# Performance work log

Hardware: AMD Instinct MI355X
Metric: run time of the kernel (lower is better)

The kernel has to match this reference:

```python
import jax, jax.numpy as jnp
import numpy as np

WEIGHT = 1.0  # config['weight']


def setup_inputs() -> dict:
    key = jax.random.key(0)
    ks = jax.random.split(key, 10)
    B, N, S, C, D, E, H, V = 8, 4096, 512, 16, 1024, 256, 1024, 100000
    return {
        "span_vecs": jax.random.normal(ks[0], (B, N, D), jnp.float32),
        "ent_table": jax.random.normal(ks[1], (V, E), jnp.float32) * 0.02,
        "W1": jax.random.normal(ks[2], (D + E, H), jnp.float32) * (1.0 / np.sqrt(D + E)),
        "b1": jnp.zeros((H,), jnp.float32),
        "W2": jax.random.normal(ks[3], (H,), jnp.float32) * (1.0 / np.sqrt(H)),
        "b2": jnp.zeros((), jnp.float32),
        "targets_all": jax.random.uniform(ks[4], (B, N, C), jnp.float32),
        "linker_indices": jax.random.randint(ks[5], (B, S), 0, N, jnp.int32),
        "candidates_all": jax.random.randint(ks[6], (B, N, C), 0, V, jnp.int32),
        "candidate_lengths_all": jax.random.randint(ks[7], (B, N), 0, C + 1, jnp.int32),
    }


def reference(span_vecs, ent_table, W1, b1, W2, b2, targets_all,
              linker_indices, candidates_all, candidate_lengths_all):
    D = span_vecs.shape[-1]
    C = candidates_all.shape[-1]
    idx = linker_indices  # [B, S]

    # batched_index_select gathers over the span axis
    candidates = jnp.take_along_axis(candidates_all, idx[:, :, None], axis=1)        # [B,S,C] int
    lengths = jnp.take_along_axis(candidate_lengths_all, idx, axis=1)                # [B,S] int
    targets = jnp.take_along_axis(targets_all, idx[:, :, None], axis=1)              # [B,S,C]
    linker_vecs = jnp.take_along_axis(span_vecs, idx[:, :, None], axis=1)            # [B,S,D]

    cand_vecs = ent_table[candidates]                                                # [B,S,C,E]

    # layers: Linear(D+E,H) -> ReLU -> (dropout=identity in eval) -> Linear(H,1)
    # fused: split W1 so the [B,S,C,D+E] expanded concat is never materialized
    W1s, W1e = W1[:D], W1[D:]
    h_span = jnp.einsum('bsd,dh->bsh', linker_vecs, W1s)                             # [B,S,H]
    h_cand = jnp.einsum('bsce,eh->bsch', cand_vecs, W1e)                             # [B,S,C,H]
    h = jax.nn.relu(h_span[:, :, None, :] + h_cand + b1)
    scores = jnp.einsum('bsch,h->bsc', h, W2) + b2                                   # [B,S,C]

    # create_candidate_mask
    mask = (jnp.arange(C)[None, None, :] < lengths[:, :, None]).astype(scores.dtype)

    # BCEWithLogitsLoss(reduction='none'), masked sum * weight
    bce = jnp.maximum(scores, 0.0) - scores * targets + jnp.log1p(jnp.exp(-jnp.abs(scores)))
    loss = (mask * bce).sum() * WEIGHT

    predictions = jnp.argmax(scores - (1.0 - mask) * 1e23, axis=-1)                  # [B,S]
    return loss, scores, predictions
```

## Files before the change

kernel.cpp:

```cpp
#include <hip/hip_runtime.h>
#include <math.h>


typedef short short8 __attribute__((ext_vector_type(8)));
typedef _Float16 half8v __attribute__((ext_vector_type(8)));
typedef float f32x16 __attribute__((ext_vector_type(16)));

static __device__ inline unsigned short f2bf(float x) {
  unsigned u = __float_as_uint(x);
  unsigned r = (u + 0x7FFFu + ((u >> 16) & 1u)) >> 16;
  return (unsigned short)r;
}
static __device__ inline float bf2f(unsigned short b) {
  return __uint_as_float(((unsigned)b) << 16);
}
static __device__ inline unsigned short f2h(float x) {
  _Float16 h = (_Float16)x;
  return *(unsigned short*)&h;
}

#define GLD_TO_LDS(gp, lp)                                          \
  __builtin_amdgcn_global_load_lds(                                 \
      (const __attribute__((address_space(1))) void*)(gp),          \
      (__attribute__((address_space(3))) void*)(lp), 16, 0, 0)

static __device__ inline void split_write(unsigned short* buf, int g,
                                          float4 c0, float4 c1) {
  float xs[8] = {c0.x, c0.y, c0.z, c0.w, c1.x, c1.y, c1.z, c1.w};
  short8 h8, l8;
#pragma unroll
  for (int j = 0; j < 8; ++j) {
    unsigned short h = f2bf(xs[j]);
    h8[j] = (short)h;
    l8[j] = (short)f2bf(xs[j] - bf2f(h));
  }
  *(short8*)(buf + (g << 3)) = h8;
  *(short8*)(buf + 4096 + (g << 3)) = l8;
}

__global__ __launch_bounds__(256) void k_prep_e(
    const float* __restrict__ ent, const float* __restrict__ W1,
    const int* __restrict__ linker, const int* __restrict__ cand_all,
    unsigned short* __restrict__ A2, unsigned short* __restrict__ sThi,
    unsigned short* __restrict__ sTlo, unsigned short* __restrict__ eT16) {
  __shared__ float t[32][33];
  const int bx = blockIdx.x;
  if (bx < 16384) {
    int f = bx * 256 + threadIdx.x;
    int row = f >> 6;
    int pair = row >> 4;
    int b = pair >> 9;
    int i = linker[pair];
    int cid = cand_all[(((size_t)b << 12) + (size_t)i) * 16 + (row & 15)];
    const float4 v = *((const float4*)(ent + ((size_t)cid << 8)) + (f & 63));
    *(ushort4*)(A2 + ((size_t)f << 2)) =
        make_ushort4(f2h(v.x), f2h(v.y), f2h(v.z), f2h(v.w));
  } else {
    int b2x = bx - 16384;
    int n0 = (b2x & 31) * 32, k0 = (b2x >> 5) * 32;
    int rr = threadIdx.x >> 5, cc = threadIdx.x & 31;
#pragma unroll
    for (int i = 0; i < 4; ++i)
      t[rr + 8 * i][cc] = W1[(size_t)(k0 + rr + 8 * i) * 1024 + n0 + cc];
    __syncthreads();
#pragma unroll
    for (int i = 0; i < 4; ++i) {
      int nl = rr + 8 * i;
      float v = t[cc][nl];
      int n = n0 + nl, k = k0 + cc;
      if (k0 < 1024) {
        unsigned short h = f2bf(v);
        unsigned short l = f2bf(v - bf2f(h));
        sThi[(size_t)n * 1024 + k] = h;
        sTlo[(size_t)n * 1024 + k] = l;
      } else {
        eT16[(size_t)n * 256 + (k - 1024)] = f2h(v);
      }
    }
  }
}

template <int KSTEPS>
__global__ __launch_bounds__(256, 2) void k_g32g(
    const float* __restrict__ span, const int* __restrict__ linker,
    const unsigned short* __restrict__ Bhi, const unsigned short* __restrict__ Blo,
    float* __restrict__ Out) {
  const int tid = threadIdx.x;
  const int l = tid & 63;
  const int w = tid >> 6;
  const int wm = w >> 1, wn = w & 1;
  const int id = blockIdx.x;
  const int z = id >> 8;
  const int sid = id & 255;
  const int m8 = sid & 7;
  const int cb = (sid >> 3) & 7;
  const int q = sid >> 6;
  const int row0 = ((q << 3) + m8) << 7;
  const int col0 = cb << 7;
  const int koff = z * (KSTEPS * 32);
  Out += (size_t)z * 4194304;

  __shared__ unsigned short lds[32768];

  f32x16 acc[2][2];
#pragma unroll
  for (int i = 0; i < 2; ++i)
#pragma unroll
    for (int j = 0; j < 2; ++j)
#pragma unroll
      for (int k = 0; k < 16; ++k) acc[i][j][k] = 0.f;

  const int ar0 = tid >> 2, ap0 = tid & 3;
  const int al0c = ap0 ^ ((ar0 >> 1) & 3);
  const int ar1 = ar0 + 64;
  const int al1c = ap0 ^ ((ar1 >> 1) & 3);
  const int r0g = row0 + ar0, r1g = row0 + ar1;
  const float* asrc0 =
      span + (((size_t)(r0g >> 9) << 12) + linker[r0g]) * 1024 + koff + al0c * 8;
  const float* asrc1 =
      span + (((size_t)(r1g >> 9) << 12) + linker[r1g]) * 1024 + koff + al1c * 8;
  const size_t boff0 = (size_t)(col0 + ar0) * 1024 + al0c * 8 + koff;
  const size_t boff1 = (size_t)(col0 + ar1) * 1024 + al1c * 8 + koff;
  const int w512 = w * 512;

  {
    float4 a00 = *(const float4*)(asrc0);
    float4 a01 = *(const float4*)(asrc0 + 4);
    float4 a10 = *(const float4*)(asrc1);
    float4 a11 = *(const float4*)(asrc1 + 4);
    GLD_TO_LDS(Bhi + boff0, lds + 8192 + w512);
    GLD_TO_LDS(Bhi + boff1, lds + 10240 + w512);
    GLD_TO_LDS(Blo + boff0, lds + 12288 + w512);
    GLD_TO_LDS(Blo + boff1, lds + 14336 + w512);
    split_write(lds, tid, a00, a01);
    split_write(lds, tid + 256, a10, a11);
  }
  asm volatile("s_waitcnt vmcnt(0) lgkmcnt(0)" ::: "memory");
  __builtin_amdgcn_s_barrier();
  asm volatile("" ::: "memory");

  for (int ks = 0; ks < KSTEPS; ++ks) {
    float4 a00, a01, a10, a11;
    const int k0n = (ks + 1) * 32;
    unsigned short* bn = lds + (((ks + 1) & 1) << 14);
    if (ks + 1 < KSTEPS) {
      a00 = *(const float4*)(asrc0 + k0n);
      a01 = *(const float4*)(asrc0 + k0n + 4);
      a10 = *(const float4*)(asrc1 + k0n);
      a11 = *(const float4*)(asrc1 + k0n + 4);
      GLD_TO_LDS(Bhi + boff0 + k0n, bn + 8192 + w512);
      GLD_TO_LDS(Bhi + boff1 + k0n, bn + 10240 + w512);
      GLD_TO_LDS(Blo + boff0 + k0n, bn + 12288 + w512);
      GLD_TO_LDS(Blo + boff1 + k0n, bn + 14336 + w512);
    }

    const unsigned short* cbuf = lds + ((ks & 1) << 14);
#pragma unroll
    for (int kc = 0; kc < 2; ++kc) {
      const int kg = kc * 2 + (l >> 5);
      short8 ah[2], alv[2], bh[2], bl[2];
#pragma unroll
      for (int it = 0; it < 2; ++it) {
        int r = wm * 64 + it * 32 + (l & 31);
        int off = r * 32 + ((kg ^ ((r >> 1) & 3)) << 3);
        ah[it] = *(const short8*)(cbuf + off);
        alv[it] = *(const short8*)(cbuf + 4096 + off);
      }
#pragma unroll
      for (int jt = 0; jt < 2; ++jt) {
        int r = wn * 64 + jt * 32 + (l & 31);
        int off = r * 32 + ((kg ^ ((r >> 1) & 3)) << 3);
        bh[jt] = *(const short8*)(cbuf + 8192 + off);
        bl[jt] = *(const short8*)(cbuf + 12288 + off);
      }
#pragma unroll
      for (int it = 0; it < 2; ++it)
#pragma unroll
        for (int jt = 0; jt < 2; ++jt) {
          acc[it][jt] = __builtin_amdgcn_mfma_f32_32x32x16_bf16(
              ah[it], bh[jt], acc[it][jt], 0, 0, 0);
          acc[it][jt] = __builtin_amdgcn_mfma_f32_32x32x16_bf16(
              ah[it], bl[jt], acc[it][jt], 0, 0, 0);
          acc[it][jt] = __builtin_amdgcn_mfma_f32_32x32x16_bf16(
              alv[it], bh[jt], acc[it][jt], 0, 0, 0);
        }
    }

    if (ks + 1 < KSTEPS) {
      split_write(bn, tid, a00, a01);
      split_write(bn, tid + 256, a10, a11);
      asm volatile("s_waitcnt vmcnt(0) lgkmcnt(0)" ::: "memory");
      __builtin_amdgcn_s_barrier();
      asm volatile("" ::: "memory");
    }
  }

#pragma unroll
  for (int it = 0; it < 2; ++it) {
    int mb = row0 + wm * 64 + it * 32 + 4 * (l >> 5);
#pragma unroll
    for (int jt = 0; jt < 2; ++jt) {
      int n = col0 + wn * 64 + jt * 32 + (l & 31);
#pragma unroll
      for (int rg = 0; rg < 16; ++rg) {
        int m = mb + (rg & 3) + 8 * (rg >> 2);
        Out[(size_t)m * 1024 + n] = acc[it][jt][rg];
      }
    }
  }
}

__global__ __launch_bounds__(256, 4) void k_gf16(
    const unsigned short* __restrict__ A,
    const unsigned short* __restrict__ Bt,
    const float* __restrict__ HsIn, const float* __restrict__ b1,
    const float* __restrict__ W2, float* __restrict__ Out) {
  const int tid = threadIdx.x;
  const int l = tid & 63;
  const int w = tid >> 6;
  const int wm = w >> 1, wn = w & 1;
  const int id = blockIdx.x;
  const int m8 = id & 7;
  const int cb = (id >> 3) & 7;
  const int q = id >> 6;
  const int row0 = ((q << 3) + m8) << 7;
  const int col0 = cb << 7;

  __shared__ unsigned short lds[16384];

  f32x16 acc[2][2];
#pragma unroll
  for (int i = 0; i < 2; ++i)
#pragma unroll
    for (int j = 0; j < 2; ++j)
#pragma unroll
      for (int k = 0; k < 16; ++k) acc[i][j][k] = 0.f;

  const int ar0 = tid >> 2, ap0 = tid & 3;
  const int al0c = ap0 ^ ((ar0 >> 1) & 3);
  const int ar1 = (tid + 256) >> 2;
  const int al1c = ap0 ^ ((ar1 >> 1) & 3);
  const size_t aoff0 = (size_t)(row0 + ar0) * 256 + al0c * 8;
  const size_t aoff1 = (size_t)(row0 + ar1) * 256 + al1c * 8;
  const size_t boff0 = (size_t)(col0 + ar0) * 256 + al0c * 8;
  const size_t boff1 = (size_t)(col0 + ar1) * 256 + al1c * 8;
  const int w512 = w * 512;

  GLD_TO_LDS(A + aoff0, lds + w512);
  GLD_TO_LDS(A + aoff1, lds + 2048 + w512);
  GLD_TO_LDS(Bt + boff0, lds + 4096 + w512);
  GLD_TO_LDS(Bt + boff1, lds + 6144 + w512);
  asm volatile("s_waitcnt vmcnt(0)" ::: "memory");
  __builtin_amdgcn_s_barrier();
  asm volatile("" ::: "memory");

#pragma unroll 2
  for (int ks = 0; ks < 8; ++ks) {
    if (ks + 1 < 8) {
      const int k0 = (ks + 1) * 32;
      unsigned short* b = lds + (((ks + 1) & 1) << 13);
      GLD_TO_LDS(A + aoff0 + k0, b + w512);
      GLD_TO_LDS(A + aoff1 + k0, b + 2048 + w512);
      GLD_TO_LDS(Bt + boff0 + k0, b + 4096 + w512);
      GLD_TO_LDS(Bt + boff1 + k0, b + 6144 + w512);
    }

    const unsigned short* cbuf = lds + ((ks & 1) << 13);
#pragma unroll
    for (int kc = 0; kc < 2; ++kc) {
      const int kg = kc * 2 + (l >> 5);
      half8v av[2], bv[2];
#pragma unroll
      for (int it = 0; it < 2; ++it) {
        int r = wm * 64 + it * 32 + (l & 31);
        int off = r * 32 + ((kg ^ ((r >> 1) & 3)) << 3);
        av[it] = *(const half8v*)(cbuf + off);
      }
#pragma unroll
      for (int jt = 0; jt < 2; ++jt) {
        int r = wn * 64 + jt * 32 + (l & 31);
        int off = r * 32 + ((kg ^ ((r >> 1) & 3)) << 3);
        bv[jt] = *(const half8v*)(cbuf + 4096 + off);
      }
#pragma unroll
      for (int it = 0; it < 2; ++it)
#pragma unroll
        for (int jt = 0; jt < 2; ++jt)
          acc[it][jt] = __builtin_amdgcn_mfma_f32_32x32x16_f16(
              av[it], bv[jt], acc[it][jt], 0, 0, 0);
    }

    if (ks + 1 < 8) {
      asm volatile("s_waitcnt vmcnt(0)" ::: "memory");
      __builtin_amdgcn_s_barrier();
      asm volatile("" ::: "memory");
    }
  }

  float sv[2][16];
#pragma unroll
  for (int it = 0; it < 2; ++it) {
#pragma unroll
    for (int rg = 0; rg < 16; ++rg) sv[it][rg] = 0.f;
    const int p0 = (row0 + wm * 64 + it * 32) >> 4;
#pragma unroll
    for (int jt = 0; jt < 2; ++jt) {
      int n = col0 + wn * 64 + jt * 32 + (l & 31);
      float b1v = b1[n], w2v = W2[n];
      float add0 = HsIn[(size_t)p0 * 1024 + n] +
                   HsIn[4194304 + (size_t)p0 * 1024 + n] + b1v;
      float add1 = HsIn[(size_t)(p0 + 1) * 1024 + n] +
                   HsIn[4194304 + (size_t)(p0 + 1) * 1024 + n] + b1v;
#pragma unroll
      for (int rg = 0; rg < 16; ++rg) {
        float h = fmaxf(acc[it][jt][rg] + (rg < 8 ? add0 : add1), 0.f);
        sv[it][rg] = fmaf(h, w2v, sv[it][rg]);
      }
    }
  }
  __syncthreads();
  float* scf = (float*)lds;
  const int cc0 = l & 31, lh4 = 4 * (l >> 5);
#pragma unroll
  for (int it = 0; it < 2; ++it)
#pragma unroll
    for (int rg = 0; rg < 16; ++rg) {
      int row = (rg & 3) + 8 * (rg >> 2) + lh4;
      scf[((w * 2 + it) * 32 + row) * 32 + ((cc0 + row) & 31)] = sv[it][rg];
    }
  __syncthreads();
  int gr = tid >> 1, h = tid & 1;
  int r = gr & 31, itv = (gr >> 5) & 1, wmv = gr >> 6;
  const float* sa = scf + ((wmv * 4 + itv) * 32 + r) * 32;
  const float* sb = scf + ((wmv * 4 + 2 + itv) * 32 + r) * 32;
  float sum = 0.f;
#pragma unroll
  for (int j = 0; j < 16; ++j) {
    int cidx = (h * 16 + j + r) & 31;
    sum += sa[cidx] + sb[cidx];
  }
  sum += __shfl_xor(sum, 1, 64);
  if (h == 0) Out[(size_t)cb * 65536 + row0 + gr] = sum;
}

__global__ __launch_bounds__(64) void k_final8(const float* __restrict__ score8,
                                               const float* __restrict__ b2p,
                                               const float* __restrict__ targets_all,
                                               const int* __restrict__ linker,
                                               const int* __restrict__ len_all,
                                               float* __restrict__ out) {
  int p = blockIdx.x * 64 + threadIdx.x;
  float b2 = b2p[0];
  int b = p >> 9;
  int i = linker[p];
  int len = len_all[(b << 12) + i];
  const float* tg = targets_all + ((((size_t)b << 12) + (size_t)i) << 4);

  float sc[16];
#pragma unroll
  for (int c = 0; c < 16; ++c) sc[c] = b2;
#pragma unroll
  for (int c8 = 0; c8 < 8; ++c8) {
    const float4* q4 = (const float4*)(score8 + (size_t)c8 * 65536 + p * 16);
#pragma unroll
    for (int j = 0; j < 4; ++j) {
      float4 v = q4[j];
      sc[j * 4 + 0] += v.x; sc[j * 4 + 1] += v.y;
      sc[j * 4 + 2] += v.z; sc[j * 4 + 3] += v.w;
    }
  }

  float loss = 0.f;
  float best = -INFINITY;
  int bc = 0;
#pragma unroll
  for (int c = 0; c < 16; ++c) {
    float s = sc[c];
    out[1 + p * 16 + c] = s;
    float val;
    if (c < len) {
      float t = tg[c];
      loss += fmaxf(s, 0.f) - s * t + log1pf(expf(-fabsf(s)));
      val = s;
    } else {
      val = s - 1e23f;
    }
    if (val > best) { best = val; bc = c; }
  }
  out[1 + 65536 + p] = (float)bc;

  for (int off = 32; off > 0; off >>= 1) loss += __shfl_down(loss, off, 64);
  if (threadIdx.x == 0) atomicAdd(out, loss);
}

#define BM 128
#define BN 128
#define BK 16
#define PAD 4

__global__ __launch_bounds__(256) void k_prep(const int* __restrict__ linker,
                                              const int* __restrict__ cand_all,
                                              int* __restrict__ cand_ids) {
  int g = blockIdx.x * 256 + threadIdx.x;
  int pair = g >> 4;
  int c = g & 15;
  int b = pair >> 9;
  int i = linker[pair];
  cand_ids[g] = cand_all[(((size_t)b << 12) + (size_t)i) * 16 + c];
}

__global__ __launch_bounds__(256) void k_hs(const float* __restrict__ span,
                                            const float* __restrict__ W1,
                                            const int* __restrict__ linker,
                                            float* __restrict__ Hs) {
  const int tid = threadIdx.x;
  const int tx = tid & 15, ty = tid >> 4;
  const int row0 = blockIdx.y * BM;
  const int col0 = blockIdx.x * BN;
  __shared__ float As[BK][BM + PAD];
  __shared__ float Bs[BK][BN + PAD];
  __shared__ int rows_g[BM];
  if (tid < BM) {
    int m = row0 + tid;
    int b = m >> 9;
    rows_g[tid] = (b << 12) + linker[m];
  }
  __syncthreads();
  float acc[8][8] = {};
  for (int k0 = 0; k0 < 1024; k0 += BK) {
#pragma unroll
    for (int ll = 0; ll < 2; ++ll) {
      int f = tid + ll * 256;
      int r = f >> 2;
      int kk = (f & 3) << 2;
      const float4 v = *(const float4*)(span + (size_t)rows_g[r] * 1024 + k0 + kk);
      As[kk + 0][r] = v.x; As[kk + 1][r] = v.y;
      As[kk + 2][r] = v.z; As[kk + 3][r] = v.w;
    }
#pragma unroll
    for (int ll = 0; ll < 2; ++ll) {
      int f = tid + ll * 256;
      int kk = f >> 5;
      int nn = (f & 31) << 2;
      *(float4*)&Bs[kk][nn] = *(const float4*)(W1 + (size_t)(k0 + kk) * 1024 + col0 + nn);
    }
    __syncthreads();
#pragma unroll
    for (int k = 0; k < BK; ++k) {
      float a[8], b[8];
      *(float4*)&a[0] = *(const float4*)&As[k][ty * 8];
      *(float4*)&a[4] = *(const float4*)&As[k][ty * 8 + 4];
      *(float4*)&b[0] = *(const float4*)&Bs[k][tx * 8];
      *(float4*)&b[4] = *(const float4*)&Bs[k][tx * 8 + 4];
#pragma unroll
      for (int i = 0; i < 8; ++i)
#pragma unroll
        for (int j = 0; j < 8; ++j) acc[i][j] = fmaf(a[i], b[j], acc[i][j]);
    }
    __syncthreads();
  }
#pragma unroll
  for (int i = 0; i < 8; ++i) {
    int m = row0 + ty * 8 + i;
    float* dst = Hs + (size_t)m * 1024 + col0 + tx * 8;
    *(float4*)dst = *(float4*)&acc[i][0];
    *(float4*)(dst + 4) = *(float4*)&acc[i][4];
  }
}

__global__ __launch_bounds__(256) void k_hc(const float* __restrict__ ent,
                                            const float* __restrict__ W1,
                                            const int* __restrict__ cand_ids,
                                            const float* __restrict__ Hs,
                                            const float* __restrict__ b1,
                                            const float* __restrict__ W2,
                                            float* __restrict__ score_ws) {
  const int tid = threadIdx.x;
  const int tx = tid & 15, ty = tid >> 4;
  const int row0 = blockIdx.y * BM;
  const int col0 = blockIdx.x * BN;
  __shared__ float As[BK][BM + PAD];
  __shared__ float Bs[BK][BN + PAD];
  __shared__ int rows_g[BM];
  __shared__ float red[BM][17];
  if (tid < BM) rows_g[tid] = cand_ids[row0 + tid];
  __syncthreads();
  float acc[8][8] = {};
  for (int k0 = 0; k0 < 256; k0 += BK) {
#pragma unroll
    for (int ll = 0; ll < 2; ++ll) {
      int f = tid + ll * 256;
      int r = f >> 2;
      int kk = (f & 3) << 2;
      const float4 v = *(const float4*)(ent + (size_t)rows_g[r] * 256 + k0 + kk);
      As[kk + 0][r] = v.x; As[kk + 1][r] = v.y;
      As[kk + 2][r] = v.z; As[kk + 3][r] = v.w;
    }
#pragma unroll
    for (int ll = 0; ll < 2; ++ll) {
      int f = tid + ll * 256;
      int kk = f >> 5;
      int nn = (f & 31) << 2;
      *(float4*)&Bs[kk][nn] =
          *(const float4*)(W1 + (size_t)(1024 + k0 + kk) * 1024 + col0 + nn);
    }
    __syncthreads();
#pragma unroll
    for (int k = 0; k < BK; ++k) {
      float a[8], b[8];
      *(float4*)&a[0] = *(const float4*)&As[k][ty * 8];
      *(float4*)&a[4] = *(const float4*)&As[k][ty * 8 + 4];
      *(float4*)&b[0] = *(const float4*)&Bs[k][tx * 8];
      *(float4*)&b[4] = *(const float4*)&Bs[k][tx * 8 + 4];
#pragma unroll
      for (int i = 0; i < 8; ++i)
#pragma unroll
        for (int j = 0; j < 8; ++j) acc[i][j] = fmaf(a[i], b[j], acc[i][j]);
    }
    __syncthreads();
  }
  const int pair = (row0 + ty * 8) >> 4;
  float hsv[8], b1v[8], w2v[8];
  {
    const float* hp = Hs + (size_t)pair * 1024 + col0 + tx * 8;
    *(float4*)&hsv[0] = *(const float4*)hp;
    *(float4*)&hsv[4] = *(const float4*)(hp + 4);
    const float* bp = b1 + col0 + tx * 8;
    *(float4*)&b1v[0] = *(const float4*)bp;
    *(float4*)&b1v[4] = *(const float4*)(bp + 4);
    const float* wp = W2 + col0 + tx * 8;
    *(float4*)&w2v[0] = *(const float4*)wp;
    *(float4*)&w2v[4] = *(const float4*)(wp + 4);
  }
#pragma unroll
  for (int i = 0; i < 8; ++i) {
    float s = 0.f;
#pragma unroll
    for (int j = 0; j < 8; ++j) {
      float h = acc[i][j] + hsv[j] + b1v[j];
      h = fmaxf(h, 0.f);
      s = fmaf(h, w2v[j], s);
    }
    red[ty * 8 + i][tx] = s;
  }
  __syncthreads();
  if (tid < BM) {
    float s = 0.f;
#pragma unroll
    for (int x = 0; x < 16; ++x) s += red[tid][x];
    atomicAdd(&score_ws[row0 + tid], s);
  }
}

__global__ __launch_bounds__(256) void k_final(const float* __restrict__ score_ws,
                                               const float* __restrict__ b2p,
                                               const float* __restrict__ targets_all,
                                               const int* __restrict__ linker,
                                               const int* __restrict__ len_all,
                                               float* __restrict__ out) {
  int p = blockIdx.x * 256 + threadIdx.x;
  float b2 = b2p[0];
  int b = p >> 9;
  int i = linker[p];
  int len = len_all[(b << 12) + i];
  const float* tg = targets_all + ((((size_t)b << 12) + (size_t)i) << 4);

  float loss = 0.f;
  float best = -INFINITY;
  int bc = 0;
#pragma unroll
  for (int c = 0; c < 16; ++c) {
    float sc = score_ws[p * 16 + c] + b2;
    out[1 + p * 16 + c] = sc;
    float val;
    if (c < len) {
      float t = tg[c];
      loss += fmaxf(sc, 0.f) - sc * t + log1pf(expf(-fabsf(sc)));
      val = sc;
    } else {
      val = sc - 1e23f;
    }
    if (val > best) { best = val; bc = c; }
  }
  out[1 + 65536 + p] = (float)bc;

  for (int off = 32; off > 0; off >>= 1) loss += __shfl_down(loss, off, 64);
  if ((threadIdx.x & 63) == 0) atomicAdd(out, loss);
}

extern "C" void kernel_launch(void* const* d_in, const int* in_sizes, int n_in,
                              void* d_out, int out_size, void* d_ws,
                              size_t ws_size, hipStream_t stream) {
  const float* span    = (const float*)d_in[0];
  const float* ent     = (const float*)d_in[1];
  const float* W1      = (const float*)d_in[2];
  const float* b1      = (const float*)d_in[3];
  const float* W2      = (const float*)d_in[4];
  const float* b2      = (const float*)d_in[5];
  const float* targets = (const float*)d_in[6];
  const int* linker    = (const int*)d_in[7];
  const int* cand_all  = (const int*)d_in[8];
  const int* len_all   = (const int*)d_in[9];
  float* out = (float*)d_out;

  char* ws = (char*)d_ws;
  float* Hs       = (float*)(ws + 0);
  float* score8   = (float*)(ws + 33554432);
  unsigned short* A2   = (unsigned short*)(ws + 35651584);
  unsigned short* sTh  = (unsigned short*)(ws + 69206016);
  unsigned short* sTl  = (unsigned short*)(ws + 71303168);
  unsigned short* eT16 = (unsigned short*)(ws + 73400320);
  float* score_ws = (float*)(ws + 73924608);
  int* cand_ids   = (int*)(ws + 74186752);
  const size_t NEED_MFMA = 74448896;

  hipMemsetAsync(d_out, 0, sizeof(float), stream);

  if (ws_size >= NEED_MFMA) {
    k_prep_e<<<dim3(17664), dim3(256), 0, stream>>>(
        ent, W1, linker, cand_all, A2, sTh, sTl, eT16);
    k_g32g<16><<<dim3(512), dim3(256), 0, stream>>>(span, linker, sTh, sTl, Hs);
    k_gf16<<<dim3(4096), dim3(256), 0, stream>>>(A2, eT16, Hs, b1, W2, score8);
    k_final8<<<dim3(64), dim3(64), 0, stream>>>(score8, b2, targets, linker,
                                                len_all, out);
  } else {
    hipMemsetAsync(score_ws, 0, 65536 * sizeof(float), stream);
    k_prep<<<dim3(256), dim3(256), 0, stream>>>(linker, cand_all, cand_ids);
    dim3 g1(8, 32);
    k_hs<<<g1, dim3(256), 0, stream>>>(span, W1, linker, Hs);
    dim3 g2(8, 512);
    k_hc<<<g2, dim3(256), 0, stream>>>(ent, W1, cand_ids, Hs, b1, W2, score_ws);
    k_final<<<dim3(16), dim3(256), 0, stream>>>(score_ws, b2, targets, linker,
                                                len_all, out);
  }
}
```

Measured before the change: 342.8 us.

## Enlarge k_gf16 block tile to 256x128 with 4x1 warp layout

The fp16 MFMA GEMM kernel now computes a 256-row by 128-column tile per block instead of 128x128. Each warp owns 64 rows across the full 128 columns, using 2x4 accumulator tiles, and the grid is halved. The goal is more arithmetic per LDS and global load, so each B tile is reused across more rows and less staging traffic is needed. The cost is more accumulator registers and LDS per block, so occupancy drops to 3 blocks per CU and there are fewer blocks to fill the GPU. The final row reduction is simplified to one thread per row.

```diff
diff --git a/kernel.cpp b/kernel.cpp
--- a/kernel.cpp
+++ b/kernel.cpp
@@ -210,7 +210,7 @@
   }
 }
 
-__global__ __launch_bounds__(256, 4) void k_gf16(
+__global__ __launch_bounds__(256, 3) void k_gf16(
     const unsigned short* __restrict__ A,
     const unsigned short* __restrict__ Bt,
     const float* __restrict__ HsIn, const float* __restrict__ b1,
@@ -218,38 +218,40 @@
   const int tid = threadIdx.x;
   const int l = tid & 63;
   const int w = tid >> 6;
-  const int wm = w >> 1, wn = w & 1;
   const int id = blockIdx.x;
   const int m8 = id & 7;
   const int cb = (id >> 3) & 7;
   const int q = id >> 6;
-  const int row0 = ((q << 3) + m8) << 7;
+  const int row0 = ((q << 3) + m8) << 8;
   const int col0 = cb << 7;
 
-  __shared__ unsigned short lds[16384];
-
-  f32x16 acc[2][2];
+  __shared__ unsigned short lds[24576];
+
+  f32x16 acc[2][4];
 #pragma unroll
   for (int i = 0; i < 2; ++i)
 #pragma unroll
-    for (int j = 0; j < 2; ++j)
+    for (int j = 0; j < 4; ++j)
 #pragma unroll
       for (int k = 0; k < 16; ++k) acc[i][j][k] = 0.f;
 
-  const int ar0 = tid >> 2, ap0 = tid & 3;
-  const int al0c = ap0 ^ ((ar0 >> 1) & 3);
-  const int ar1 = (tid + 256) >> 2;
-  const int al1c = ap0 ^ ((ar1 >> 1) & 3);
-  const size_t aoff0 = (size_t)(row0 + ar0) * 256 + al0c * 8;
-  const size_t aoff1 = (size_t)(row0 + ar1) * 256 + al1c * 8;
-  const size_t boff0 = (size_t)(col0 + ar0) * 256 + al0c * 8;
-  const size_t boff1 = (size_t)(col0 + ar1) * 256 + al1c * 8;
+  const int ar = tid >> 2, ap = tid & 3;
+  const int ac = ap ^ ((ar >> 1) & 3);
+  const size_t abase = (size_t)(row0 + ar) * 256 + ac * 8;
+  const size_t bbase = (size_t)(col0 + ar) * 256 + ac * 8;
   const int w512 = w * 512;
 
-  GLD_TO_LDS(A + aoff0, lds + w512);
-  GLD_TO_LDS(A + aoff1, lds + 2048 + w512);
-  GLD_TO_LDS(Bt + boff0, lds + 4096 + w512);
-  GLD_TO_LDS(Bt + boff1, lds + 6144 + w512);
+#define STAGE2(buf, ks32)                                        \
+  do {                                                           \
+    GLD_TO_LDS(A + abase + (ks32), (buf) + w512);                \
+    GLD_TO_LDS(A + abase + 16384 + (ks32), (buf) + 2048 + w512); \
+    GLD_TO_LDS(A + abase + 32768 + (ks32), (buf) + 4096 + w512); \
+    GLD_TO_LDS(A + abase + 49152 + (ks32), (buf) + 6144 + w512); \
+    GLD_TO_LDS(Bt + bbase + (ks32), (buf) + 8192 + w512);        \
+    GLD_TO_LDS(Bt + bbase + 16384 + (ks32), (buf) + 10240 + w512);\
+  } while (0)
+
+  STAGE2(lds, 0);
   asm volatile("s_waitcnt vmcnt(0)" ::: "memory");
   __builtin_amdgcn_s_barrier();
   asm volatile("" ::: "memory");
@@ -257,35 +259,31 @@
 #pragma unroll 2
   for (int ks = 0; ks < 8; ++ks) {
     if (ks + 1 < 8) {
-      const int k0 = (ks + 1) * 32;
-      unsigned short* b = lds + (((ks + 1) & 1) << 13);
-      GLD_TO_LDS(A + aoff0 + k0, b + w512);
-      GLD_TO_LDS(A + aoff1 + k0, b + 2048 + w512);
-      GLD_TO_LDS(Bt + boff0 + k0, b + 4096 + w512);
-      GLD_TO_LDS(Bt + boff1 + k0, b + 6144 + w512);
-    }
-
-    const unsigned short* cbuf = lds + ((ks & 1) << 13);
+      unsigned short* bn = lds + ((ks + 1) & 1) * 12288;
+      STAGE2(bn, (ks + 1) * 32);
+    }
+
+    const unsigned short* cbuf = lds + (ks & 1) * 12288;
 #pragma unroll
     for (int kc = 0; kc < 2; ++kc) {
       const int kg = kc * 2 + (l >> 5);
-      half8v av[2], bv[2];
+      half8v av[2], bv[4];
 #pragma unroll
       for (int it = 0; it < 2; ++it) {
-        int r = wm * 64 + it * 32 + (l & 31);
+        int r = w * 64 + it * 32 + (l & 31);
         int off = r * 32 + ((kg ^ ((r >> 1) & 3)) << 3);
         av[it] = *(const half8v*)(cbuf + off);
       }
 #pragma unroll
-      for (int jt = 0; jt < 2; ++jt) {
-        int r = wn * 64 + jt * 32 + (l & 31);
-        int off = r * 32 + ((kg ^ ((r >> 1) & 3)) << 3);
-        bv[jt] = *(const half8v*)(cbuf + 4096 + off);
+      for (int jt = 0; jt < 4; ++jt) {
+        int r = jt * 32 + (l & 31);
+        int off = 8192 + r * 32 + ((kg ^ ((r >> 1) & 3)) << 3);
+        bv[jt] = *(const half8v*)(cbuf + off);
       }
 #pragma unroll
       for (int it = 0; it < 2; ++it)
 #pragma unroll
-        for (int jt = 0; jt < 2; ++jt)
+        for (int jt = 0; jt < 4; ++jt)
           acc[it][jt] = __builtin_amdgcn_mfma_f32_32x32x16_f16(
               av[it], bv[jt], acc[it][jt], 0, 0, 0);
     }
@@ -296,16 +294,17 @@
       asm volatile("" ::: "memory");
     }
   }
+#undef STAGE2
 
   float sv[2][16];
 #pragma unroll
   for (int it = 0; it < 2; ++it) {
 #pragma unroll
     for (int rg = 0; rg < 16; ++rg) sv[it][rg] = 0.f;
-    const int p0 = (row0 + wm * 64 + it * 32) >> 4;
-#pragma unroll
-    for (int jt = 0; jt < 2; ++jt) {
-      int n = col0 + wn * 64 + jt * 32 + (l & 31);
+    const int p0 = (row0 + w * 64 + it * 32) >> 4;
+#pragma unroll
+    for (int jt = 0; jt < 4; ++jt) {
+      int n = col0 + jt * 32 + (l & 31);
       float b1v = b1[n], w2v = W2[n];
       float add0 = HsIn[(size_t)p0 * 1024 + n] +
                    HsIn[4194304 + (size_t)p0 * 1024 + n] + b1v;
@@ -329,18 +328,13 @@
       scf[((w * 2 + it) * 32 + row) * 32 + ((cc0 + row) & 31)] = sv[it][rg];
     }
   __syncthreads();
-  int gr = tid >> 1, h = tid & 1;
-  int r = gr & 31, itv = (gr >> 5) & 1, wmv = gr >> 6;
-  const float* sa = scf + ((wmv * 4 + itv) * 32 + r) * 32;
-  const float* sb = scf + ((wmv * 4 + 2 + itv) * 32 + r) * 32;
+  int gr = tid;
+  int wv = gr >> 6, itv = (gr >> 5) & 1, r = gr & 31;
+  const float* srow = scf + ((wv * 2 + itv) * 32 + r) * 32;
   float sum = 0.f;
 #pragma unroll
-  for (int j = 0; j < 16; ++j) {
-    int cidx = (h * 16 + j + r) & 31;
-    sum += sa[cidx] + sb[cidx];
-  }
-  sum += __shfl_xor(sum, 1, 64);
-  if (h == 0) Out[(size_t)cb * 65536 + row0 + gr] = sum;
+  for (int j = 0; j < 32; ++j) sum += srow[(j + r) & 31];
+  Out[(size_t)cb * 65536 + row0 + gr] = sum;
 }
 
 __global__ __launch_bounds__(64) void k_final8(const float* __restrict__ score8,
@@ -620,7 +614,7 @@
     k_prep_e<<<dim3(17664), dim3(256), 0, stream>>>(
         ent, W1, linker, cand_all, A2, sTh, sTl, eT16);
     k_g32g<16><<<dim3(512), dim3(256), 0, stream>>>(span, linker, sTh, sTl, Hs);
-    k_gf16<<<dim3(4096), dim3(256), 0, stream>>>(A2, eT16, Hs, b1, W2, score8);
+    k_gf16<<<dim3(2048), dim3(256), 0, stream>>>(A2, eT16, Hs, b1, W2, score8);
     k_final8<<<dim3(64), dim3(64), 0, stream>>>(score8, b2, targets, linker,
                                                 len_all, out);
   } else {
```

After: 330.9 us. 1.04x faster.
